# Optimization experiments

Measured on AMD Instinct MI355X. Metric: run time of the kernel, lower is better.

The kernel has to match this reference:

```python
import jax, jax.numpy as jnp
import numpy as np

FRAME_SIZE = 80
PITCH_MIN = 32
PITCH_MAX = 300
RADIUS = 2


def setup_inputs() -> dict:
    key = jax.random.key(0)
    k1, k2 = jax.random.split(key)
    B, C, F = 64, 1, 4000
    x = jax.random.normal(k1, (B, C, FRAME_SIZE * F), dtype=jnp.float32)
    # valid period range so lookup indices stay in-bounds (p <= PITCH_MAX - RADIUS)
    periods = jax.random.randint(k2, (B, F), 0, 299)
    return {"x": x, "periods": periods}


def reference(x, periods):
    B, C, N = x.shape          # C must be 1 (as required by torch.gather in original)
    F = periods.shape[1]
    W = 2 * RADIUS + 1
    offs = jnp.arange(-RADIUS, RADIUS + 1)          # [W]
    idx = jnp.arange(N)                              # [N]
    # repeat_interleave(periods, frame_size, dim=1) -> per-sample period
    p_up = jnp.repeat(periods, FRAME_SIZE, axis=1)   # [B, N]
    lookup = idx[None, :] + PITCH_MAX - p_up         # [B, N]
    lookup = lookup[:, :, None] + offs               # [B, N, W]
    x_pad = jnp.pad(x, ((0, 0), (0, 0), (PITCH_MAX, 0)))  # [B, C, N+PITCH_MAX]
    xs = x_pad[:, 0, :]                              # [B, N+PITCH_MAX]
    # gather lagged samples (no materialization of the repeated x_ext tensor)
    x_select = xs[jnp.arange(B)[:, None, None], lookup]   # [B, N, W]
    x_frames = x.reshape(B, C, F, FRAME_SIZE, 1)
    lag_frames = x_select.reshape(B, 1, F, FRAME_SIZE, W)
    dotp = jnp.sum(x_frames * lag_frames, axis=-2)         # [B, C, F, W]
    frame_nrg = jnp.sum(x_frames * x_frames, axis=-2)      # [B, C, F, 1]
    lag_nrg = jnp.sum(lag_frames * lag_frames, axis=-2)    # [B, 1, F, W]
    acorr = dotp / jnp.sqrt(frame_nrg * lag_nrg + 1e-9)
    return acorr
```

## Files before the change

### kernel.cpp

```cpp
#include <hip/hip_runtime.h>

namespace {
constexpr int kFrame = 80;
constexpr int kRad   = 2;
constexpr int kW     = 5;
constexpr int kB     = 64;
constexpr int kF     = 4000;
constexpr int kN     = kFrame * kF;

constexpr int FPB     = 64;
constexpr int BPB     = (kF + FPB - 1) / FPB;
constexpr int HALO_LO = 304;
constexpr int HALO_HI = 84;
constexpr int LN      = FPB * kFrame + HALO_LO + HALO_HI;
constexpr int LPHYS   = LN + 4 * ((LN + 31) / 32);
constexpr int NQ      = 6;
}

__device__ __forceinline__ int phys(int i) { return i + ((i >> 5) << 2); }

__device__ __forceinline__ float qsum(float v) {
    v += __int_as_float(__builtin_amdgcn_mov_dpp(__float_as_int(v), 0xB1, 0xF, 0xF, true));
    v += __int_as_float(__builtin_amdgcn_mov_dpp(__float_as_int(v), 0x4E, 0xF, 0xF, true));
    return v;
}

template <bool SAFE>
__device__ __forceinline__ void issue_stage(const float* __restrict__ xb, int o,
                                            int tid, float4* r) {
#pragma unroll
    for (int k = 0; k < NQ; ++k) {
        int i4 = (k * 256 + tid) * 4;
        if (i4 < LN) {
            if constexpr (SAFE) {
                r[k] = *reinterpret_cast<const float4*>(xb + o + i4);
            } else {
                int g = o + i4;
                float t0 = (g + 0 >= 0) ? xb[min(g + 0, kN - 1)] : 0.f;
                float t1 = (g + 1 >= 0) ? xb[min(g + 1, kN - 1)] : 0.f;
                float t2 = (g + 2 >= 0) ? xb[min(g + 2, kN - 1)] : 0.f;
                float t3 = (g + 3 >= 0) ? xb[min(g + 3, kN - 1)] : 0.f;
                r[k] = make_float4(t0, t1, t2, t3);
            }
        }
    }
}

__device__ __forceinline__ void write_stage(float* __restrict__ buf, int tid,
                                            const float4* r) {
#pragma unroll
    for (int k = 0; k < NQ; ++k) {
        int i4 = (k * 256 + tid) * 4;
        if (i4 < LN)
            *reinterpret_cast<float4*>(&buf[phys(i4)]) = r[k];
    }
}

__global__ __launch_bounds__(256, 4)
void pitch_acorr_kernel(const float* __restrict__ x,
                        const int* __restrict__ periods,
                        float* __restrict__ out) {
    __shared__ float lds[LPHYS];

    const int bid = blockIdx.x;
    const int b   = bid / BPB;
    const int blk = bid - b * BPB;
    const int f0  = blk * FPB;
    const int nf  = min(FPB, kF - f0);
    const int tid = threadIdx.x;
    const int fl  = tid >> 2;
    const int q   = tid & 3;
    const int h   = q * 20;
    const float* xb = x + (long long)b * kN;
    const int o = f0 * kFrame - HALO_LO;

    const int p = periods[b * kF + min(f0 + fl, kF - 1)];

    float4 r[NQ];
    const bool safe = (o >= 0) && (o + LN <= kN);
    if (safe) issue_stage<true >(xb, o, tid, r);
    else      issue_stage<false>(xb, o, tid, r);

    const int frameg = (f0 + fl) * kFrame + h;
    float4 Fa, Fb, Fc, Fd, Fe;
    {
        const float* fb_ = xb;
        Fa = *reinterpret_cast<const float4*>(fb_ + min(frameg +  0, kN - 4));
        Fb = *reinterpret_cast<const float4*>(fb_ + min(frameg +  4, kN - 4));
        Fc = *reinterpret_cast<const float4*>(fb_ + min(frameg +  8, kN - 4));
        Fd = *reinterpret_cast<const float4*>(fb_ + min(frameg + 12, kN - 4));
        Fe = *reinterpret_cast<const float4*>(fb_ + min(frameg + 16, kN - 4));
    }

    write_stage(lds, tid, r);
    __syncthreads();

    if (fl >= nf) return;

    const int fbase = fl * kFrame + HALO_LO;
    const int lbase = fbase - p - kRad;
    const int s     = lbase & 3;
    const int A0    = lbase - s;
    const int gst   = A0 + h;

#define LD4(i) (*reinterpret_cast<const float4*>(&lds[phys(i)]))
    const float4 Ga = LD4(gst +  0), Gb = LD4(gst +  4), Gc = LD4(gst +  8),
                 Gd = LD4(gst + 12), Ge = LD4(gst + 16), Gf = LD4(gst + 20),
                 Gg = LD4(gst + 24);
#undef LD4

    const float g0 = Ga.x, g1 = Ga.y, g2 = Ga.z, g3 = Ga.w,
                g4 = Gb.x, g5 = Gb.y, g6 = Gb.z, g7 = Gb.w,
                g8 = Gc.x, g9 = Gc.y, g10 = Gc.z, g11 = Gc.w,
                g12 = Gd.x, g13 = Gd.y, g14 = Gd.z, g15 = Gd.w,
                g16 = Ge.x, g17 = Ge.y, g18 = Ge.z, g19 = Ge.w,
                g20 = Gf.x, g21 = Gf.y, g22 = Gf.z, g23 = Gf.w,
                g24 = Gg.x, g25 = Gg.y, g26 = Gg.z;

    const float E0 = g0*g0 + g1*g1 + g2*g2 + g3*g3 + g4*g4 + g5*g5 + g6*g6
                   + g7*g7 + g8*g8 + g9*g9 + g10*g10 + g11*g11 + g12*g12
                   + g13*g13 + g14*g14 + g15*g15 + g16*g16 + g17*g17 + g18*g18
                   + g19*g19;

    float fn = 0.f;
    float D0 = 0.f, D1 = 0.f, D2 = 0.f, D3 = 0.f,
          D4 = 0.f, D5 = 0.f, D6 = 0.f, D7 = 0.f;

#define STEP(FT, A, B, C, D, E, F, G, H)                                       \
    { const float ft = (FT);                                                   \
      fn += ft * ft;                                                           \
      D0 += ft * (A); D1 += ft * (B); D2 += ft * (C); D3 += ft * (D);          \
      D4 += ft * (E); D5 += ft * (F); D6 += ft * (G); D7 += ft * (H); }

    STEP(Fa.x, g0, g1, g2, g3, g4, g5, g6, g7)
    STEP(Fa.y, g1, g2, g3, g4, g5, g6, g7, g8)
    STEP(Fa.z, g2, g3, g4, g5, g6, g7, g8, g9)
    STEP(Fa.w, g3, g4, g5, g6, g7, g8, g9, g10)
    STEP(Fb.x, g4, g5, g6, g7, g8, g9, g10, g11)
    STEP(Fb.y, g5, g6, g7, g8, g9, g10, g11, g12)
    STEP(Fb.z, g6, g7, g8, g9, g10, g11, g12, g13)
    STEP(Fb.w, g7, g8, g9, g10, g11, g12, g13, g14)
    STEP(Fc.x, g8, g9, g10, g11, g12, g13, g14, g15)
    STEP(Fc.y, g9, g10, g11, g12, g13, g14, g15, g16)
    STEP(Fc.z, g10, g11, g12, g13, g14, g15, g16, g17)
    STEP(Fc.w, g11, g12, g13, g14, g15, g16, g17, g18)
    STEP(Fd.x, g12, g13, g14, g15, g16, g17, g18, g19)
    STEP(Fd.y, g13, g14, g15, g16, g17, g18, g19, g20)
    STEP(Fd.z, g14, g15, g16, g17, g18, g19, g20, g21)
    STEP(Fd.w, g15, g16, g17, g18, g19, g20, g21, g22)
    STEP(Fe.x, g16, g17, g18, g19, g20, g21, g22, g23)
    STEP(Fe.y, g17, g18, g19, g20, g21, g22, g23, g24)
    STEP(Fe.z, g18, g19, g20, g21, g22, g23, g24, g25)
    STEP(Fe.w, g19, g20, g21, g22, g23, g24, g25, g26)
#undef STEP

    const float E1 = E0 + (g20*g20 - g0*g0);
    const float E2 = E1 + (g21*g21 - g1*g1);
    const float E3 = E2 + (g22*g22 - g2*g2);
    const float E4 = E3 + (g23*g23 - g3*g3);
    const float E5 = E4 + (g24*g24 - g4*g4);
    const float E6 = E5 + (g25*g25 - g5*g5);
    const float E7 = E6 + (g26*g26 - g6*g6);

    const bool s1 = (s & 1) != 0, s2 = (s & 2) != 0;
    float d0 = s2 ? (s1 ? D3 : D2) : (s1 ? D1 : D0);
    float d1 = s2 ? (s1 ? D4 : D3) : (s1 ? D2 : D1);
    float d2 = s2 ? (s1 ? D5 : D4) : (s1 ? D3 : D2);
    float d3 = s2 ? (s1 ? D6 : D5) : (s1 ? D4 : D3);
    float d4 = s2 ? (s1 ? D7 : D6) : (s1 ? D5 : D4);
    float e0 = s2 ? (s1 ? E3 : E2) : (s1 ? E1 : E0);
    float e1 = s2 ? (s1 ? E4 : E3) : (s1 ? E2 : E1);
    float e2 = s2 ? (s1 ? E5 : E4) : (s1 ? E3 : E2);
    float e3 = s2 ? (s1 ? E6 : E5) : (s1 ? E4 : E3);
    float e4 = s2 ? (s1 ? E7 : E6) : (s1 ? E5 : E4);

    fn = qsum(fn);
    d0 = qsum(d0); d1 = qsum(d1); d2 = qsum(d2); d3 = qsum(d3); d4 = qsum(d4);
    e0 = qsum(e0); e1 = qsum(e1); e2 = qsum(e2); e3 = qsum(e3); e4 = qsum(e4);

    float* op = out + (long long)(b * kF + f0 + fl) * kW;
    const float dq = (q & 2) ? ((q & 1) ? d3 : d2) : ((q & 1) ? d1 : d0);
    const float eq = (q & 2) ? ((q & 1) ? e3 : e2) : ((q & 1) ? e1 : e0);
    op[q] = dq * rsqrtf(fn * eq + 1e-9f);
    if (q == 0) op[4] = d4 * rsqrtf(fn * e4 + 1e-9f);
}

extern "C" void kernel_launch(void* const* d_in, const int* in_sizes, int n_in,
                              void* d_out, int out_size, void* d_ws, size_t ws_size,
                              hipStream_t stream) {
    const float* x       = (const float*)d_in[0];
    const int*   periods = (const int*)d_in[1];
    float*       out     = (float*)d_out;

    const int grid = kB * BPB;
    pitch_acorr_kernel<<<grid, 256, 0, stream>>>(x, periods, out);
}
```

Measured before the change: 20.90 us.

## Drop LDS staging, load lag windows directly from global with XCD-aware block mapping

Removes the shared-memory halo staging and the block barrier. Each thread now reads its lagged window straight from global memory, relying on L1/L2 to absorb the overlapping reuse. Work is flattened across batch×frames, so there are no partial tail blocks, and block IDs are remapped so neighbouring chunks land on the same XCD for L2 locality. The cost is redundant global/cache traffic for the overlapping lag windows and unaligned float4 global loads.

New measurement: 20.53 us. About the same (-1.8%).

```diff
diff --git a/kernel.cpp b/kernel.cpp
--- a/kernel.cpp
+++ b/kernel.cpp
@@ -8,16 +8,11 @@
 constexpr int kF     = 4000;
 constexpr int kN     = kFrame * kF;
 
-constexpr int FPB     = 64;
-constexpr int BPB     = (kF + FPB - 1) / FPB;
-constexpr int HALO_LO = 304;
-constexpr int HALO_HI = 84;
-constexpr int LN      = FPB * kFrame + HALO_LO + HALO_HI;
-constexpr int LPHYS   = LN + 4 * ((LN + 31) / 32);
-constexpr int NQ      = 6;
+constexpr int FPB   = 64;
+constexpr int NBLK  = (kB * kF) / FPB;
+constexpr int NXCD  = 8;
+constexpr int CPX   = NBLK / NXCD;
 }
-
-__device__ __forceinline__ int phys(int i) { return i + ((i >> 5) << 2); }
 
 __device__ __forceinline__ float qsum(float v) {
     v += __int_as_float(__builtin_amdgcn_mov_dpp(__float_as_int(v), 0xB1, 0xF, 0xF, true));
@@ -25,96 +20,70 @@
     return v;
 }
 
-template <bool SAFE>
-__device__ __forceinline__ void issue_stage(const float* __restrict__ xb, int o,
-                                            int tid, float4* r) {
-#pragma unroll
-    for (int k = 0; k < NQ; ++k) {
-        int i4 = (k * 256 + tid) * 4;
-        if (i4 < LN) {
-            if constexpr (SAFE) {
-                r[k] = *reinterpret_cast<const float4*>(xb + o + i4);
-            } else {
-                int g = o + i4;
-                float t0 = (g + 0 >= 0) ? xb[min(g + 0, kN - 1)] : 0.f;
-                float t1 = (g + 1 >= 0) ? xb[min(g + 1, kN - 1)] : 0.f;
-                float t2 = (g + 2 >= 0) ? xb[min(g + 2, kN - 1)] : 0.f;
-                float t3 = (g + 3 >= 0) ? xb[min(g + 3, kN - 1)] : 0.f;
-                r[k] = make_float4(t0, t1, t2, t3);
-            }
-        }
-    }
-}
-
-__device__ __forceinline__ void write_stage(float* __restrict__ buf, int tid,
-                                            const float4* r) {
-#pragma unroll
-    for (int k = 0; k < NQ; ++k) {
-        int i4 = (k * 256 + tid) * 4;
-        if (i4 < LN)
-            *reinterpret_cast<float4*>(&buf[phys(i4)]) = r[k];
-    }
+__device__ __forceinline__ float4 ld4c(const float* __restrict__ xb, int g) {
+    float t0 = (g + 0 >= 0) ? xb[min(g + 0, kN - 1)] : 0.f;
+    float t1 = (g + 1 >= 0) ? xb[min(g + 1, kN - 1)] : 0.f;
+    float t2 = (g + 2 >= 0) ? xb[min(g + 2, kN - 1)] : 0.f;
+    float t3 = (g + 3 >= 0) ? xb[min(g + 3, kN - 1)] : 0.f;
+    return make_float4(t0, t1, t2, t3);
 }
 
 __global__ __launch_bounds__(256, 4)
 void pitch_acorr_kernel(const float* __restrict__ x,
                         const int* __restrict__ periods,
                         float* __restrict__ out) {
-    __shared__ float lds[LPHYS];
-
     const int bid = blockIdx.x;
-    const int b   = bid / BPB;
-    const int blk = bid - b * BPB;
-    const int f0  = blk * FPB;
-    const int nf  = min(FPB, kF - f0);
+    const int wid = (bid & (NXCD - 1)) * CPX + (bid >> 3);
     const int tid = threadIdx.x;
     const int fl  = tid >> 2;
     const int q   = tid & 3;
     const int h   = q * 20;
+
+    const int gf = wid * FPB + fl;
+    const int b  = gf / kF;
+    const int f  = gf - b * kF;
     const float* xb = x + (long long)b * kN;
-    const int o = f0 * kFrame - HALO_LO;
 
-    const int p = periods[b * kF + min(f0 + fl, kF - 1)];
+    const int p = periods[gf];
 
-    float4 r[NQ];
-    const bool safe = (o >= 0) && (o + LN <= kN);
-    if (safe) issue_stage<true >(xb, o, tid, r);
-    else      issue_stage<false>(xb, o, tid, r);
+    const int fst = f * kFrame + h;
+    const float4 Fa = *reinterpret_cast<const float4*>(xb + fst +  0);
+    const float4 Fb = *reinterpret_cast<const float4*>(xb + fst +  4);
+    const float4 Fc = *reinterpret_cast<const float4*>(xb + fst +  8);
+    const float4 Fd = *reinterpret_cast<const float4*>(xb + fst + 12);
+    const float4 Fe = *reinterpret_cast<const float4*>(xb + fst + 16);
 
-    const int frameg = (f0 + fl) * kFrame + h;
-    float4 Fa, Fb, Fc, Fd, Fe;
-    {
-        const float* fb_ = xb;
-        Fa = *reinterpret_cast<const float4*>(fb_ + min(frameg +  0, kN - 4));
-        Fb = *reinterpret_cast<const float4*>(fb_ + min(frameg +  4, kN - 4));
-        Fc = *reinterpret_cast<const float4*>(fb_ + min(frameg +  8, kN - 4));
-        Fd = *reinterpret_cast<const float4*>(fb_ + min(frameg + 12, kN - 4));
-        Fe = *reinterpret_cast<const float4*>(fb_ + min(frameg + 16, kN - 4));
-    }
-
-    write_stage(lds, tid, r);
-    __syncthreads();
-
-    if (fl >= nf) return;
-
-    const int fbase = fl * kFrame + HALO_LO;
-    const int lbase = fbase - p - kRad;
+    const int lbase = f * kFrame - p - kRad;
     const int s     = lbase & 3;
     const int A0    = lbase - s;
     const int gst   = A0 + h;
 
-#define LD4(i) (*reinterpret_cast<const float4*>(&lds[phys(i)]))
-    const float4 Ga = LD4(gst +  0), Gb = LD4(gst +  4), Gc = LD4(gst +  8),
-                 Gd = LD4(gst + 12), Ge = LD4(gst + 16), Gf = LD4(gst + 20),
-                 Gg = LD4(gst + 24);
-#undef LD4
+    float4 Ga, Gb, Gc, Gd, Ge, Gf_, Gg;
+    const bool safe = (A0 >= 0) && (A0 + 88 <= kN);
+    if (safe) {
+        Ga = *reinterpret_cast<const float4*>(xb + gst +  0);
+        Gb = *reinterpret_cast<const float4*>(xb + gst +  4);
+        Gc = *reinterpret_cast<const float4*>(xb + gst +  8);
+        Gd = *reinterpret_cast<const float4*>(xb + gst + 12);
+        Ge = *reinterpret_cast<const float4*>(xb + gst + 16);
+        Gf_= *reinterpret_cast<const float4*>(xb + gst + 20);
+        Gg = *reinterpret_cast<const float4*>(xb + gst + 24);
+    } else {
+        Ga = ld4c(xb, gst +  0);
+        Gb = ld4c(xb, gst +  4);
+        Gc = ld4c(xb, gst +  8);
+        Gd = ld4c(xb, gst + 12);
+        Ge = ld4c(xb, gst + 16);
+        Gf_= ld4c(xb, gst + 20);
+        Gg = ld4c(xb, gst + 24);
+    }
 
     const float g0 = Ga.x, g1 = Ga.y, g2 = Ga.z, g3 = Ga.w,
                 g4 = Gb.x, g5 = Gb.y, g6 = Gb.z, g7 = Gb.w,
                 g8 = Gc.x, g9 = Gc.y, g10 = Gc.z, g11 = Gc.w,
                 g12 = Gd.x, g13 = Gd.y, g14 = Gd.z, g15 = Gd.w,
                 g16 = Ge.x, g17 = Ge.y, g18 = Ge.z, g19 = Ge.w,
-                g20 = Gf.x, g21 = Gf.y, g22 = Gf.z, g23 = Gf.w,
+                g20 = Gf_.x, g21 = Gf_.y, g22 = Gf_.z, g23 = Gf_.w,
                 g24 = Gg.x, g25 = Gg.y, g26 = Gg.z;
 
     const float E0 = g0*g0 + g1*g1 + g2*g2 + g3*g3 + g4*g4 + g5*g5 + g6*g6
@@ -178,7 +147,7 @@
     d0 = qsum(d0); d1 = qsum(d1); d2 = qsum(d2); d3 = qsum(d3); d4 = qsum(d4);
     e0 = qsum(e0); e1 = qsum(e1); e2 = qsum(e2); e3 = qsum(e3); e4 = qsum(e4);
 
-    float* op = out + (long long)(b * kF + f0 + fl) * kW;
+    float* op = out + (long long)gf * kW;
     const float dq = (q & 2) ? ((q & 1) ? d3 : d2) : ((q & 1) ? d1 : d0);
     const float eq = (q & 2) ? ((q & 1) ? e3 : e2) : ((q & 1) ? e1 : e0);
     op[q] = dq * rsqrtf(fn * eq + 1e-9f);
@@ -192,6 +161,5 @@
     const int*   periods = (const int*)d_in[1];
     float*       out     = (float*)d_out;
 
-    const int grid = kB * BPB;
-    pitch_acorr_kernel<<<grid, 256, 0, stream>>>(x, periods, out);
+    pitch_acorr_kernel<<<NBLK, 256, 0, stream>>>(x, periods, out);
 }
```
